# Optimization experiments

Hardware: AMD Instinct MI355X
Metric: run time of the kernel (lower is better)

Reference implementation:

```python
import jax, jax.numpy as jnp
import numpy as np
from jax import lax

RATIO = 2.0
ITERATIONS = 1


def setup_inputs() -> dict:
    key = jax.random.key(0)
    k1, k2 = jax.random.split(key)
    N, H, W = 64, 512, 512
    x = jax.random.normal(k1, (N, H, W), dtype=jnp.float32)  # logits
    y = jax.random.randint(k2, (N, H, W), 0, 2, dtype=jnp.int32)  # binary labels
    return {"x": x, "y": y}


def _erode(m):
    # cv2.erode with 3x3 all-ones kernel == 3x3 min-pool; cv2 default border
    # value for erode is +inf, matching reduce_window's init_value padding.
    return lax.reduce_window(m, jnp.inf, lax.min, (1, 3, 3), (1, 1, 1), 'SAME')


def _dilate(m):
    # cv2.dilate == 3x3 max-pool; default border value -inf == init_value pad.
    return lax.reduce_window(m, -jnp.inf, lax.max, (1, 3, 3), (1, 1, 1), 'SAME')


def reference(x, y):
    yf = y.astype(x.dtype)
    # elementwise BCE-with-logits (reduction='none'), numerically stable
    loss = jnp.maximum(x, 0.0) - x * yf + jnp.log1p(jnp.exp(-jnp.abs(x)))
    m = (y > 0).astype(x.dtype)  # [N,H,W] binary mask
    ero, dil = m, m
    for _ in range(ITERATIONS):
        ero = _erode(ero)
        dil = _dilate(dil)
    border = dil - ero  # 1 on border pixels, 0 elsewhere
    w = border * RATIO + (1.0 - border)
    return (loss * w).mean()
```

## Files before the change

kernel.cpp:

```cpp
#include <hip/hip_runtime.h>
#include <math.h>

#define NIMG 64
#define HH 512
#define WW 512
#define TR 8
#define SPI (HH / TR)
#define NSTRIP (NIMG * SPI)
#define WPB 4
#define NBLK (NSTRIP / WPB)
#define INV_TOTAL (1.0f / 16777216.0f)

typedef unsigned int u32;
typedef unsigned long long u64;

__device__ __forceinline__ u32 packy(const int4 v) {
    const u32 lo = __builtin_amdgcn_perm((u32)v.y, (u32)v.x, 0x0c0c0400u);
    const u32 hi = __builtin_amdgcn_perm((u32)v.w, (u32)v.z, 0x04000c0cu);
    return 0x02020202u - (lo | hi);
}

__device__ __forceinline__ u64 hor3v(u32 flo, u32 fhi, u32 mL, u32 mR) {
    const u32 lw = __shfl_up(fhi, 1);
    const u32 rw = __shfl_down(flo, 1);
    const u64 f = (u64)flo | ((u64)fhi << 32);
    u64 h = f | (f << 8) | (f >> 8);
    h |= (u64)((lw >> 24) & mL);
    h |= ((u64)((rw << 24) & mR)) << 32;
    return h;
}

__device__ __forceinline__ void px4(const float4 xv, const u32 mb, const u32 bb,
                                    float& accA, float& accB)
{
    { const float s = xv.x * fmaf((float)(mb & 0xffu), -2.0f, 1.0f);
      const float t = fmaxf(s, 0.0f) + __logf(1.0f + __expf(-fabsf(s)));
      accA += t; accB = fmaf(t, (float)(bb & 0xffu), accB); }
    { const float s = xv.y * fmaf((float)((mb >> 8) & 0xffu), -2.0f, 1.0f);
      const float t = fmaxf(s, 0.0f) + __logf(1.0f + __expf(-fabsf(s)));
      accA += t; accB = fmaf(t, (float)((bb >> 8) & 0xffu), accB); }
    { const float s = xv.z * fmaf((float)((mb >> 16) & 0xffu), -2.0f, 1.0f);
      const float t = fmaxf(s, 0.0f) + __logf(1.0f + __expf(-fabsf(s)));
      accA += t; accB = fmaf(t, (float)((bb >> 16) & 0xffu), accB); }
    { const float s = xv.w * fmaf((float)(mb >> 24), -2.0f, 1.0f);
      const float t = fmaxf(s, 0.0f) + __logf(1.0f + __expf(-fabsf(s)));
      accA += t; accB = fmaf(t, (float)(bb >> 24), accB); }
}

__global__ __launch_bounds__(256, 4) void border_loss_main(
    const float* __restrict__ x, const int* __restrict__ y,
    float* __restrict__ part, int atomic_mode)
{
    __shared__ float wsum[WPB];

    const int tid  = threadIdx.x;
    const int lane = tid & 63;
    const int wv   = tid >> 6;
    const int s    = blockIdx.x * WPB + wv;
    const int n    = s >> 6;
    const int R0   = (s & (SPI - 1)) * TR;
    const int*   __restrict__ yimg = y + n * (HH * WW);
    const float* __restrict__ ximg = x + n * (HH * WW);

    const u32 mL = (lane == 0)  ? 0u : 0xffu;
    const u32 mR = (lane == 63) ? 0u : 0xff000000u;

    const u32 offBase = (u32)(R0 * WW + (lane << 3));
    const u32 offYMax = (u32)((HH - 1) * WW + (lane << 3));

    const int4* q;
    q = (const int4*)(yimg + (offBase - ((R0 > 0) ? WW : 0)));
    int4 tm0 = q[0], tm1 = q[1];
    q = (const int4*)(yimg + offBase);
    int4 t00 = q[0], t01 = q[1];
    q = (const int4*)(yimg + (offBase + WW));
    int4 y10 = q[0], y11 = q[1];
    q = (const int4*)(yimg + (offBase + 2 * WW));
    int4 y00 = q[0], y01 = q[1];
    const float4* qx;
    qx = (const float4*)(ximg + offBase);
    float4 x00 = qx[0], x01 = qx[1];
    qx = (const float4*)(ximg + (offBase + WW));
    float4 x10 = qx[0], x11 = qx[1];

    u32 alo = packy(tm0), ahi = packy(tm1);
    if (R0 == 0) { alo = 0u; ahi = 0u; }
    u64 hau = hor3v(alo, ahi, mL, mR);
    const u32 blo = packy(t00), bhi = packy(t01);
    u64 hbu = hor3v(blo, bhi, mL, mR);
    u64 fbu = (u64)blo | ((u64)bhi << 32);

    u32 offY = offBase + 3 * WW;
    u32 offX = offBase + 2 * WW;

    float accA = 0.0f, accB = 0.0f;

    #define BODY(YA, YB, XA, XB, KILL, ISSUE)                                  \
    {                                                                          \
        u32 flo = packy(YA);                                                   \
        u32 fhi = packy(YB);                                                   \
        if (KILL) { flo = 0u; fhi = 0u; }        \
        const u64 hcu = hor3v(flo, fhi, mL, mR);                               \
        if (ISSUE) {                             \
            const u32 oy = (offY < offYMax) ? offY : offYMax;                  \
            const int4* pp = (const int4*)(yimg + oy);                         \
            YA = pp[0]; YB = pp[1];                                            \
            offY += WW;                                                        \
        }                                                                      \
        const u64 v  = hau | hbu | hcu;                                        \
        const u64 bd = v & (v >> 1) & 0x0101010101010101ull;                   \
        const u32 m_lo = (u32)fbu & 0x01010101u;                               \
        const u32 m_hi = (u32)(fbu >> 32) & 0x01010101u;                       \
        px4(XA, m_lo, (u32)bd, accA, accB);                                    \
        px4(XB, m_hi, (u32)(bd >> 32), accA, accB);                            \
        if (ISSUE) {                             \
            const float4* px = (const float4*)(ximg + offX);                   \
            XA = px[0]; XB = px[1];                                            \
            offX += WW;                                                        \
        }                                                                      \
        hau = hbu; hbu = hcu; fbu = (u64)flo | ((u64)fhi << 32);               \
    }

    #pragma unroll 1
    for (int it = 0; it < TR; it += 2) {
        BODY(y10, y11, x00, x01, false, (it < TR - 2));
        BODY(y00, y01, x10, x11, (R0 + it + 2 >= HH), (it + 1 < TR - 2));
    }
    #undef BODY

    float acc = accA + accB;
    #pragma unroll
    for (int off = 32; off > 0; off >>= 1)
        acc += __shfl_down(acc, off);
    if (lane == 0) wsum[wv] = acc;
    __syncthreads();
    if (tid == 0) {
        const float t = wsum[0] + wsum[1] + wsum[2] + wsum[3];
        if (atomic_mode) atomicAdd(part, t * INV_TOTAL);
        else             part[blockIdx.x] = t;
    }
}

__global__ __launch_bounds__(256) void border_loss_reduce(
    const float* __restrict__ part, float* __restrict__ out)
{
    __shared__ float wsum[4];
    float t = 0.0f;
    for (int i = threadIdx.x; i < NBLK; i += 256) t += part[i];
    #pragma unroll
    for (int off = 32; off > 0; off >>= 1)
        t += __shfl_down(t, off);
    if ((threadIdx.x & 63) == 0) wsum[threadIdx.x >> 6] = t;
    __syncthreads();
    if (threadIdx.x == 0)
        out[0] = (wsum[0] + wsum[1] + wsum[2] + wsum[3]) * INV_TOTAL;
}

__global__ void border_loss_zero(float* out) { out[0] = 0.0f; }

extern "C" void kernel_launch(void* const* d_in, const int* in_sizes, int n_in,
                              void* d_out, int out_size, void* d_ws, size_t ws_size,
                              hipStream_t stream)
{
    const float* x = (const float*)d_in[0];
    const int*   y = (const int*)d_in[1];
    float* out = (float*)d_out;

    if (ws_size >= (size_t)NBLK * sizeof(float)) {
        float* part = (float*)d_ws;
        border_loss_main<<<NBLK, 256, 0, stream>>>(x, y, part, 0);
        border_loss_reduce<<<1, 256, 0, stream>>>(part, out);
    } else {
        border_loss_zero<<<1, 1, 0, stream>>>(out);
        border_loss_main<<<NBLK, 256, 0, stream>>>(x, y, out, 1);
    }
}
```

Baseline: 148.7 us.

## Stage label strip with halo in LDS via direct global-to-LDS loads

Each block now handles a 16-row strip of one image and stages the 18 label rows (with halo) into shared memory using global_load_lds. Each wave then computes four output rows from LDS, and the x loads are issued up front. The aim is to cut the redundant halo label reads from global memory and replace the per-wave serial row-streaming pipeline with a bulk LDS staging step. In exchange it uses about 36KB of LDS per block, which may limit occupancy, and it adds a block barrier before any compute can start.

After: 147.1 us, median of 2. About the same (-1.1%).

```diff
diff --git a/kernel.cpp b/kernel.cpp
--- a/kernel.cpp
+++ b/kernel.cpp
@@ -4,34 +4,33 @@
 #define NIMG 64
 #define HH 512
 #define WW 512
-#define TR 8
-#define SPI (HH / TR)
-#define NSTRIP (NIMG * SPI)
-#define WPB 4
-#define NBLK (NSTRIP / WPB)
+#define TR 16
+#define SPB (HH / TR)
+#define NBLK (NIMG * SPB)
+#define LROWS (TR + 2)
 #define INV_TOTAL (1.0f / 16777216.0f)
 
 typedef unsigned int u32;
 typedef unsigned long long u64;
+typedef __attribute__((address_space(1))) const int as1_cint;
+typedef __attribute__((address_space(3))) int       as3_int;
 
-__device__ __forceinline__ u32 packy(const int4 v) {
+__device__ __forceinline__ u32 packy4(const int4 v) {
     const u32 lo = __builtin_amdgcn_perm((u32)v.y, (u32)v.x, 0x0c0c0400u);
     const u32 hi = __builtin_amdgcn_perm((u32)v.w, (u32)v.z, 0x04000c0cu);
     return 0x02020202u - (lo | hi);
 }
 
-__device__ __forceinline__ u64 hor3v(u32 flo, u32 fhi, u32 mL, u32 mR) {
-    const u32 lw = __shfl_up(fhi, 1);
-    const u32 rw = __shfl_down(flo, 1);
-    const u64 f = (u64)flo | ((u64)fhi << 32);
-    u64 h = f | (f << 8) | (f >> 8);
-    h |= (u64)((lw >> 24) & mL);
-    h |= ((u64)((rw << 24) & mR)) << 32;
-    return h;
+__device__ __forceinline__ u32 hor3u(u32 F, u32 fL, u32 fR, int lane) {
+    const u32 up = __shfl_up(F, 1);
+    const u32 dn = __shfl_down(F, 1);
+    const u32 hL = (lane == 0)  ? fL : (up >> 24);
+    const u32 hR = (lane == 63) ? fR : (dn & 0xffu);
+    return F | (F << 8) | (F >> 8) | hL | (hR << 24);
 }
 
-__device__ __forceinline__ void px4(const float4 xv, const u32 mb, const u32 bb,
-                                    float& accA, float& accB)
+__device__ __forceinline__ void px4u(const float4 xv, const u32 mb, const u32 bb,
+                                     float& accA, float& accB)
 {
     { const float s = xv.x * fmaf((float)(mb & 0xffu), -2.0f, 1.0f);
       const float t = fmaxf(s, 0.0f) + __logf(1.0f + __expf(-fabsf(s)));
@@ -51,82 +50,83 @@
     const float* __restrict__ x, const int* __restrict__ y,
     float* __restrict__ part, int atomic_mode)
 {
-    __shared__ float wsum[WPB];
+    __shared__ int   tile[LROWS * WW];
+    __shared__ float wsum[4];
 
-    const int tid  = threadIdx.x;
-    const int lane = tid & 63;
-    const int wv   = tid >> 6;
-    const int s    = blockIdx.x * WPB + wv;
-    const int n    = s >> 6;
-    const int R0   = (s & (SPI - 1)) * TR;
+    const int tid   = threadIdx.x;
+    const int lane  = tid & 63;
+    const int wv    = tid >> 6;
+    const int b     = blockIdx.x;
+    const int n     = b >> 5;
+    const int strip = b & 31;
+    const int R0    = strip * TR;
     const int*   __restrict__ yimg = y + n * (HH * WW);
     const float* __restrict__ ximg = x + n * (HH * WW);
+    const bool topS = (strip == 0);
+    const bool botS = (strip == SPB - 1);
 
-    const u32 mL = (lane == 0)  ? 0u : 0xffu;
-    const u32 mR = (lane == 63) ? 0u : 0xff000000u;
+    #pragma unroll
+    for (int i = 0; i < 9; ++i) {
+        const int c    = (i << 2) | wv;
+        const int j    = c >> 1;
+        const int half = c & 1;
+        int g = R0 - 1 + j;
+        g = (g < 0) ? 0 : ((g > HH - 1) ? HH - 1 : g);
+        const int* src = yimg + g * WW + (half << 8) + (lane << 2);
+        __builtin_amdgcn_global_load_lds((as1_cint*)src,
+                                         (as3_int*)&tile[c << 8], 16, 0, 0);
+    }
 
-    const u32 offBase = (u32)(R0 * WW + (lane << 3));
-    const u32 offYMax = (u32)((HH - 1) * WW + (lane << 3));
+    const int r0w = R0 + (wv << 2);
+    const float* xw = ximg + r0w * WW + (lane << 2);
+    const float4 xv00 = *(const float4*)(xw + 0 * WW);
+    const float4 xv01 = *(const float4*)(xw + 0 * WW + 256);
+    const float4 xv10 = *(const float4*)(xw + 1 * WW);
+    const float4 xv11 = *(const float4*)(xw + 1 * WW + 256);
+    const float4 xv20 = *(const float4*)(xw + 2 * WW);
+    const float4 xv21 = *(const float4*)(xw + 2 * WW + 256);
+    const float4 xv30 = *(const float4*)(xw + 3 * WW);
+    const float4 xv31 = *(const float4*)(xw + 3 * WW + 256);
 
-    const int4* q;
-    q = (const int4*)(yimg + (offBase - ((R0 > 0) ? WW : 0)));
-    int4 tm0 = q[0], tm1 = q[1];
-    q = (const int4*)(yimg + offBase);
-    int4 t00 = q[0], t01 = q[1];
-    q = (const int4*)(yimg + (offBase + WW));
-    int4 y10 = q[0], y11 = q[1];
-    q = (const int4*)(yimg + (offBase + 2 * WW));
-    int4 y00 = q[0], y01 = q[1];
-    const float4* qx;
-    qx = (const float4*)(ximg + offBase);
-    float4 x00 = qx[0], x01 = qx[1];
-    qx = (const float4*)(ximg + (offBase + WW));
-    float4 x10 = qx[0], x11 = qx[1];
+    __syncthreads();
 
-    u32 alo = packy(tm0), ahi = packy(tm1);
-    if (R0 == 0) { alo = 0u; ahi = 0u; }
-    u64 hau = hor3v(alo, ahi, mL, mR);
-    const u32 blo = packy(t00), bhi = packy(t01);
-    u64 hbu = hor3v(blo, bhi, mL, mR);
-    u64 fbu = (u64)blo | ((u64)bhi << 32);
-
-    u32 offY = offBase + 3 * WW;
-    u32 offX = offBase + 2 * WW;
-
+    const int jw = wv << 2;
     float accA = 0.0f, accB = 0.0f;
 
-    #define BODY(YA, YB, XA, XB, KILL, ISSUE)                                  \
-    {                                                                          \
-        u32 flo = packy(YA);                                                   \
-        u32 fhi = packy(YB);                                                   \
-        if (KILL) { flo = 0u; fhi = 0u; }        \
-        const u64 hcu = hor3v(flo, fhi, mL, mR);                               \
-        if (ISSUE) {                             \
-            const u32 oy = (offY < offYMax) ? offY : offYMax;                  \
-            const int4* pp = (const int4*)(yimg + oy);                         \
-            YA = pp[0]; YB = pp[1];                                            \
-            offY += WW;                                                        \
-        }                                                                      \
-        const u64 v  = hau | hbu | hcu;                                        \
-        const u64 bd = v & (v >> 1) & 0x0101010101010101ull;                   \
-        const u32 m_lo = (u32)fbu & 0x01010101u;                               \
-        const u32 m_hi = (u32)(fbu >> 32) & 0x01010101u;                       \
-        px4(XA, m_lo, (u32)bd, accA, accB);                                    \
-        px4(XB, m_hi, (u32)(bd >> 32), accA, accB);                            \
-        if (ISSUE) {                             \
-            const float4* px = (const float4*)(ximg + offX);                   \
-            XA = px[0]; XB = px[1];                                            \
-            offX += WW;                                                        \
-        }                                                                      \
-        hau = hbu; hbu = hcu; fbu = (u64)flo | ((u64)fhi << 32);               \
-    }
+    #define ROWF(J, H, Fv, Hv) { \
+        const int jj = (J); \
+        const bool jvalid = !(topS && jj == 0) && !(botS && jj == LROWS - 1); \
+        const int4 yv = *(const int4*)&tile[jj * WW + ((H) << 8) + (lane << 2)]; \
+        const int  ev = tile[jj * WW + ((H) ? 255 : 256)]; \
+        u32 F = 0u, fe = 0u; \
+        if (jvalid) { F = packy4(yv); fe = 2u - (u32)ev; } \
+        (Fv) = F; \
+        (Hv) = hor3u(F, (H) ? fe : 0u, (H) ? 0u : fe, lane); }
 
-    #pragma unroll 1
-    for (int it = 0; it < TR; it += 2) {
-        BODY(y10, y11, x00, x01, false, (it < TR - 2));
-        BODY(y00, y01, x10, x11, (R0 + it + 2 >= HH), (it + 1 < TR - 2));
-    }
-    #undef BODY
+    #define OUT(HA, HB, HC, FM, XV) { \
+        const u32 V  = (HA) | (HB) | (HC); \
+        const u32 bd = V & (V >> 1) & 0x01010101u; \
+        px4u((XV), (FM) & 0x01010101u, bd, accA, accB); }
+
+    #define HALF(H, XA, XB, XC, XD) { \
+        u32 Fa, Ha, Fb, Hb, Fc, Hc; \
+        ROWF(jw,     H, Fa, Ha) \
+        ROWF(jw + 1, H, Fb, Hb) \
+        ROWF(jw + 2, H, Fc, Hc) \
+        OUT(Ha, Hb, Hc, Fb, XA) \
+        ROWF(jw + 3, H, Fa, Ha) \
+        OUT(Hb, Hc, Ha, Fc, XB) \
+        ROWF(jw + 4, H, Fb, Hb) \
+        OUT(Hc, Ha, Hb, Fa, XC) \
+        ROWF(jw + 5, H, Fc, Hc) \
+        OUT(Ha, Hb, Hc, Fb, XD) }
+
+    HALF(0, xv00, xv10, xv20, xv30)
+    HALF(1, xv01, xv11, xv21, xv31)
+
+    #undef HALF
+    #undef OUT
+    #undef ROWF
 
     float acc = accA + accB;
     #pragma unroll
```
